# Optimization experiments

Hardware: AMD Instinct MI355X
Metric: run time of the kernel (lower is better)

The kernel has to match this reference:

```python
import jax, jax.numpy as jnp
import numpy as np

NUM_EXPERTS = 32
TOP_K = 4
ALPHA = 1.702   # GPT-OSS GLU alpha
LIMIT = 7.0     # GPT-OSS clamp limit


def setup_inputs() -> dict:
    key = jax.random.key(0)
    ks = jax.random.split(key, 7)
    B, S, H, E = 2, 2048, 1024, NUM_EXPERTS
    return {
        "hidden_states": jax.random.normal(ks[0], (B, S, H), jnp.float32),
        "router_weight": jax.random.normal(ks[1], (E, H), jnp.float32) * 0.02,
        "router_bias": jax.random.normal(ks[2], (E,), jnp.float32) * 0.02,
        "gate_up_proj": jax.random.normal(ks[3], (E, H, 2 * H), jnp.float32) * 0.02,
        "gate_up_proj_bias": jax.random.normal(ks[4], (E, 2 * H), jnp.float32) * 0.02,
        "down_proj": jax.random.normal(ks[5], (E, H, H), jnp.float32) * 0.02,
        "down_proj_bias": jax.random.normal(ks[6], (E, H), jnp.float32) * 0.02,
    }


def _moe_forward(hidden_states, router_weight, router_bias,
                 gate_up_proj, gate_up_proj_bias, down_proj, down_proj_bias):
    B, S, H = hidden_states.shape
    E, K = NUM_EXPERTS, TOP_K
    T = B * S
    capacity = T * K // E * 2  # expert_capacity as in the torch module

    x = hidden_states.reshape(T, H)

    # ---- router: linear -> top-k -> softmax over top-k -> dense scatter ----
    logits = x @ router_weight.T + router_bias                     # [T, E]
    top_vals, top_idx = jax.lax.top_k(logits, K)                   # [T, K]
    weights = jax.nn.softmax(top_vals, axis=-1)                    # [T, K]
    router_scores = jnp.zeros_like(logits).at[
        jnp.arange(T)[:, None], top_idx].set(weights)              # [T, E]

    # ---- capacity-based dispatch (first-come-first-served in token order) ----
    flat_e = top_idx.reshape(-1)                                   # [T*K]
    token_id = jnp.repeat(jnp.arange(T), K)                        # [T*K]
    onehot = (flat_e[:, None] == jnp.arange(E)[None, :]).astype(jnp.int32)
    # rank of each assignment within its expert (0-based, arrival order)
    rank = jnp.take_along_axis(jnp.cumsum(onehot, axis=0),
                               flat_e[:, None], axis=1)[:, 0] - 1  # [T*K]
    valid = rank < capacity
    slot = jnp.where(valid, rank, capacity)  # out-of-range slot -> dropped

    buffer = jnp.zeros((E, capacity, H), x.dtype).at[flat_e, slot].set(
        x[token_id], mode="drop")                                  # [E, C, H]

    # ---- grouped expert MLP: gate_up GEMM + GPT-OSS GLU + down GEMM ----
    gu = jnp.einsum("ech,ehf->ecf", buffer, gate_up_proj) \
         + gate_up_proj_bias[:, None, :]                           # [E, C, 2H]
    gate = gu[..., ::2]
    up = gu[..., 1::2]
    gate = jnp.minimum(gate, LIMIT)
    up = jnp.clip(up, -LIMIT, LIMIT)
    glu = gate * jax.nn.sigmoid(gate * ALPHA)
    act = (up + 1.0) * glu                                         # [E, C, H]
    expert_out = jnp.einsum("ech,ehf->ecf", act, down_proj) \
                 + down_proj_bias[:, None, :]                      # [E, C, H]

    # ---- weighted combine (dropped tokens contribute zero) ----
    gathered = expert_out[flat_e, jnp.where(valid, rank, 0)]       # [T*K, H]
    w = router_scores[token_id, flat_e] * valid.astype(x.dtype)    # [T*K]
    out = jax.ops.segment_sum(gathered * w[:, None], token_id,
                              num_segments=T)                      # [T, H]
    return out.reshape(B, S, H), router_scores


def reference(hidden_states, router_weight, router_bias, gate_up_proj,
              gate_up_proj_bias, down_proj, down_proj_bias):
    return _moe_forward(hidden_states, router_weight, router_bias,
                        gate_up_proj, gate_up_proj_bias, down_proj,
                        down_proj_bias)
```

## Files before the change

kernel.cpp:

```cpp
#include <hip/hip_runtime.h>
#include <hip/hip_bf16.h>

#define T_TOK 4096
#define H_DIM 1024
#define E_EXP 32
#define TOPK 4
#define CAP 1024
#define PAIRS (T_TOK*TOPK)

typedef __attribute__((ext_vector_type(8))) short short8v;
typedef __attribute__((ext_vector_type(4))) short short4v;
typedef __attribute__((ext_vector_type(4))) float f32x4;
typedef unsigned long long u64;
typedef unsigned short ushort;

__device__ __forceinline__ float bf16_bits_to_f32(ushort h) {
    return __uint_as_float(((unsigned)h) << 16);
}
__device__ __forceinline__ unsigned bf16r(float f) {
    unsigned u = __float_as_uint(f);
    return ((u + 0x7fffu + ((u >> 16) & 1u)) >> 16) & 0xffffu;
}
__device__ __forceinline__ unsigned cvt2(float a, float b) {
    unsigned r;
    asm("v_cvt_pk_bf16_f32 %0, %1, %2" : "=v"(r) : "v"(a), "v"(b));
    return r;
}
__device__ __forceinline__ u64 pk4(float a, float b, float c, float d) {
    return (u64)cvt2(a, b) | ((u64)cvt2(c, d) << 32);
}

#define GLD16(gsrc, ldst) \
    __builtin_amdgcn_global_load_lds( \
        (const __attribute__((address_space(1))) unsigned*)(gsrc), \
        (__attribute__((address_space(3))) unsigned*)(ldst), 16, 0, 0)

__global__ __launch_bounds__(256) void router_kernel(
    const float* __restrict__ x, const float* __restrict__ rw,
    const float* __restrict__ rb, float* __restrict__ scores,
    int* __restrict__ flat_e, float* __restrict__ flat_w)
{
    __shared__ float xs[H_DIM];
    __shared__ float lg[E_EXP];
    __shared__ float sw[TOPK];
    __shared__ int   se[TOPK];
    const int t = blockIdx.x;
    const int tid = threadIdx.x;

    for (int i = tid; i < H_DIM; i += 256) xs[i] = x[(size_t)t * H_DIM + i];
    __syncthreads();

    const int e = tid >> 3, l8 = tid & 7;
    float partial = 0.f;
    const float* wr = rw + (size_t)e * H_DIM;
    for (int h = l8; h < H_DIM; h += 8) partial += xs[h] * wr[h];
    partial += __shfl_xor(partial, 1);
    partial += __shfl_xor(partial, 2);
    partial += __shfl_xor(partial, 4);
    if (l8 == 0) lg[e] = partial + rb[e];
    __syncthreads();

    if (tid == 0) {
        unsigned used = 0;
        float bv[TOPK]; int bi[TOPK];
        #pragma unroll
        for (int j = 0; j < TOPK; j++) {
            float best = -1e30f; int bid = -1;
            for (int q = 0; q < E_EXP; q++) {
                if (used & (1u << q)) continue;
                if (lg[q] > best) { best = lg[q]; bid = q; }
            }
            used |= 1u << bid;
            bv[j] = best; bi[j] = bid;
        }
        const float m = bv[0];
        float s = 0.f; float w[TOPK];
        #pragma unroll
        for (int j = 0; j < TOPK; j++) { w[j] = expf(bv[j] - m); s += w[j]; }
        const float inv = 1.f / s;
        #pragma unroll
        for (int j = 0; j < TOPK; j++) { sw[j] = w[j] * inv; se[j] = bi[j]; }
    }
    __syncthreads();

    if (tid < E_EXP) {
        float v = 0.f;
        #pragma unroll
        for (int j = 0; j < TOPK; j++) if (se[j] == tid) v = sw[j];
        scores[(size_t)t * E_EXP + tid] = v;
    }
    if (tid < TOPK) {
        flat_e[t * TOPK + tid] = se[tid];
        flat_w[t * TOPK + tid] = sw[tid];
    }
}

__global__ __launch_bounds__(256) void scan_kernel(
    const int* __restrict__ flat_e, const float* __restrict__ flat_w,
    int* __restrict__ slot_token, float* __restrict__ slot_w,
    int* __restrict__ pair_slot, int* __restrict__ counts)
{
    __shared__ int cnt[256 * E_EXP];
    const int tid = threadIdx.x;
    for (int e = 0; e < E_EXP; e++) cnt[tid * E_EXP + e] = 0;
    __syncthreads();
    const int base = tid * (PAIRS / 256);
    for (int i = 0; i < PAIRS / 256; i++) {
        int e = flat_e[base + i];
        cnt[tid * E_EXP + e]++;
    }
    __syncthreads();
    if (tid < E_EXP) {
        int run = 0;
        for (int i = 0; i < 256; i++) {
            int idx = i * E_EXP + tid;
            int v = cnt[idx];
            cnt[idx] = run;
            run += v;
        }
        counts[tid] = min(run, CAP);
    }
    __syncthreads();
    for (int i = 0; i < PAIRS / 256; i++) {
        int p = base + i;
        int e = flat_e[p];
        int r = cnt[tid * E_EXP + e]++;
        if (r < CAP) {
            slot_token[e * CAP + r] = p >> 2;
            slot_w[e * CAP + r] = flat_w[p];
            pair_slot[p] = r;
        } else {
            pair_slot[p] = -1;
        }
    }
}

__global__ __launch_bounds__(256) void stage_tokens(
    const float* __restrict__ x, const int* __restrict__ slot_token,
    const int* __restrict__ counts, char* __restrict__ xbuf)
{
    const int e = blockIdx.y, rt = blockIdx.x;
    const int n = counts[e];
    const int row0 = rt * 128;
    if (row0 >= n) return;
    const int rows_here = min(128, n - row0);
    const int lane = threadIdx.x & 63, wv = threadIdx.x >> 6;
    char* tb = xbuf + ((size_t)(e * 8 + rt)) * 262144;

    for (int r = wv; r < rows_here; r += 4) {
        const float* xr = x + (size_t)slot_token[e * CAP + row0 + r] * H_DIM;
        #pragma unroll
        for (int q = 0; q < 2; ++q) {
            int g = q * 64 + lane;
            float4 a = *(const float4*)(xr + g * 8);
            float4 b = *(const float4*)(xr + g * 8 + 4);
            uint4 w;
            w.x = cvt2(a.x, a.y); w.y = cvt2(a.z, a.w);
            w.z = cvt2(b.x, b.y); w.w = cvt2(b.z, b.w);
            int kb = g >> 2, gi = g & 3;
            *(uint4*)(tb + kb * 8192 + r * 64 + ((gi ^ (r & 3)) * 16)) = w;
        }
    }
}

__global__ __launch_bounds__(256, 3) void gateup_mfma(
    const char* __restrict__ xbuf,
    const float* __restrict__ wgu,
    const float* __restrict__ gub,
    const int* __restrict__ counts,
    char* __restrict__ act)
{
    const int lin = blockIdx.x;
    const int xcd = lin & 7, slot = lin >> 3;
    const int gg = (slot >> 3) * 8 + xcd;
    const int rt = slot & 7;
    const int e = gg >> 4, ct = gg & 15;

    const int n = counts[e];
    const int row0 = rt * 128;
    if (row0 >= n) return;
    const int rows_here = min(128, n - row0);
    const int c0f = ct * 64, c0gu = ct * 128;

    __shared__ char AsB[2][8192];
    __shared__ char BgB[2][4096];
    __shared__ char BuB[2][4096];

    const int tid = threadIdx.x;
    const int lane = tid & 63, wid = tid >> 6;
    const int wr = wid >> 1, wc = wid & 1;
    const int l15 = lane & 15, l4 = lane >> 4;

    const char* xtile = xbuf + ((size_t)(e * 8 + rt)) * 262144;

    f32x4 accg[4][2], accu[4][2];
    #pragma unroll
    for (int m = 0; m < 4; m++)
        #pragma unroll
        for (int j = 0; j < 2; j++) { accg[m][j] = (f32x4)0.f; accu[m][j] = (f32x4)0.f; }

    float2 bgv[2][4];
    const int bnp = tid & 63;
    const int bkq0 = tid >> 6;

    auto stageA = [&](int buf, int t) {
        const char* src = xtile + (size_t)t * 8192 + wid * 2048 + lane * 16;
        char* dst = AsB[buf] + wid * 2048;
        GLD16(src, dst);
        GLD16(src + 1024, dst + 1024);
    };
    auto bload = [&](int k0) {
        #pragma unroll
        for (int u = 0; u < 2; ++u) {
            int kq = bkq0 + 4 * u;
            const float* src = wgu + ((size_t)e * H_DIM + k0 + kq * 4) * 2048 + c0gu + 2 * bnp;
            #pragma unroll
            for (int q = 0; q < 4; ++q) bgv[u][q] = *(const float2*)(src + (size_t)q * 2048);
        }
    };
    auto bpack = [&](int buf) {
        #pragma unroll
        for (int u = 0; u < 2; ++u) {
            int kq = bkq0 + 4 * u;
            *(u64*)(BgB[buf] + kq * 512 + bnp * 8) =
                pk4(bgv[u][0].x, bgv[u][1].x, bgv[u][2].x, bgv[u][3].x);
            *(u64*)(BuB[buf] + kq * 512 + bnp * 8) =
                pk4(bgv[u][0].y, bgv[u][1].y, bgv[u][2].y, bgv[u][3].y);
        }
    };

    bload(0);
    stageA(0, 0);
    bpack(0);
    __syncthreads();
    int cur = 0;

    for (int t = 0; t < 32; ++t) {
        if (t < 31) { bload((t + 1) * 32); stageA(cur ^ 1, t + 1); }

        short8v afr[4];
        #pragma unroll
        for (int m = 0; m < 4; ++m) {
            int row = wr * 64 + m * 16 + l15;
            afr[m] = *(short8v*)(AsB[cur] + row * 64 + ((l4 ^ (row & 3)) * 16));
        }
        #pragma unroll
        for (int j = 0; j < 2; ++j) {
            int f = wc * 32 + j * 16 + l15;
            short4v glo = *(short4v*)(BgB[cur] + (2 * l4) * 512 + f * 8);
            short4v ghi = *(short4v*)(BgB[cur] + (2 * l4 + 1) * 512 + f * 8);
            short4v ulo = *(short4v*)(BuB[cur] + (2 * l4) * 512 + f * 8);
            short4v uhi = *(short4v*)(BuB[cur] + (2 * l4 + 1) * 512 + f * 8);
            short8v bg8 = __builtin_shufflevector(glo, ghi, 0, 1, 2, 3, 4, 5, 6, 7);
            short8v bu8 = __builtin_shufflevector(ulo, uhi, 0, 1, 2, 3, 4, 5, 6, 7);
            #pragma unroll
            for (int m = 0; m < 4; ++m) {
                accg[m][j] = __builtin_amdgcn_mfma_f32_16x16x32_bf16(afr[m], bg8, accg[m][j], 0, 0, 0);
                accu[m][j] = __builtin_amdgcn_mfma_f32_16x16x32_bf16(afr[m], bu8, accu[m][j], 0, 0, 0);
            }
        }
        if (t < 31) bpack(cur ^ 1);
        __syncthreads();
        cur ^= 1;
    }

    char* atile = act + ((size_t)(e * 8 + rt)) * 262144;
    #pragma unroll
    for (int j = 0; j < 2; ++j) {
        int f = c0f + wc * 32 + j * 16 + l15;
        float bgb = gub[(size_t)e * 2048 + 2 * f];
        float bub = gub[(size_t)e * 2048 + 2 * f + 1];
        int kb = f >> 5, gi = (f & 31) >> 3, ke = f & 7;
        #pragma unroll
        for (int m = 0; m < 4; ++m) {
            int rbase = wr * 64 + m * 16 + l4 * 4;
            #pragma unroll
            for (int reg = 0; reg < 4; ++reg) {
                int r = rbase + reg;
                if (r >= rows_here) continue;
                float g = accg[m][j][reg] + bgb;
                float u = accu[m][j][reg] + bub;
                g = fminf(g, 7.0f);
                u = fminf(fmaxf(u, -7.0f), 7.0f);
                float glu = g / (1.0f + __expf(-1.702f * g));
                float a = (u + 1.0f) * glu;
                *(ushort*)(atile + kb * 8192 + r * 64 + ((gi ^ (r & 3)) * 16) + ke * 2)
                    = (ushort)bf16r(a);
            }
        }
    }
}

__global__ __launch_bounds__(256, 3) void down_mfma(
    const char* __restrict__ act,
    const float* __restrict__ wd,
    const float* __restrict__ db,
    const int* __restrict__ counts,
    ushort* __restrict__ eout)
{
    const int lin = blockIdx.x;
    const int xcd = lin & 7, slot = lin >> 3;
    const int gg = (slot >> 3) * 8 + xcd;
    const int rt = slot & 7;
    const int e = gg >> 3, ct = gg & 7;

    const int n = counts[e];
    const int row0 = rt * 128;
    if (row0 >= n) return;
    const int rows_here = min(128, n - row0);
    const int c0 = ct * 128;

    __shared__ char AsB[2][8192];
    __shared__ char BsB[2][8192];

    const int tid = threadIdx.x;
    const int lane = tid & 63, wid = tid >> 6;
    const int wr = wid >> 1, wc = wid & 1;
    const int l15 = lane & 15, l4 = lane >> 4;

    const char* atile = act + ((size_t)(e * 8 + rt)) * 262144;

    f32x4 acc[4][4];
    #pragma unroll
    for (int m = 0; m < 4; m++)
        #pragma unroll
        for (int j = 0; j < 4; j++) acc[m][j] = (f32x4)0.f;

    float2 bvd[2][4];
    const int bnp = tid & 63;
    const int bkq0 = tid >> 6;

    auto stageA = [&](int buf, int t) {
        const char* src = atile + (size_t)t * 8192 + wid * 2048 + lane * 16;
        char* dst = AsB[buf] + wid * 2048;
        GLD16(src, dst);
        GLD16(src + 1024, dst + 1024);
    };
    auto bload = [&](int k0) {
        #pragma unroll
        for (int u = 0; u < 2; ++u) {
            int kq = bkq0 + 4 * u;
            const float* src = wd + ((size_t)e * H_DIM + k0 + kq * 4) * H_DIM + c0 + 2 * bnp;
            #pragma unroll
            for (int q = 0; q < 4; ++q) bvd[u][q] = *(const float2*)(src + (size_t)q * H_DIM);
        }
    };
    auto bpack = [&](int buf) {
        #pragma unroll
        for (int u = 0; u < 2; ++u) {
            int kq = bkq0 + 4 * u;
            char* dst = BsB[buf] + kq * 1024 + bnp * 16;
            *(u64*)dst       = pk4(bvd[u][0].x, bvd[u][1].x, bvd[u][2].x, bvd[u][3].x);
            *(u64*)(dst + 8) = pk4(bvd[u][0].y, bvd[u][1].y, bvd[u][2].y, bvd[u][3].y);
        }
    };

    bload(0);
    stageA(0, 0);
    bpack(0);
    __syncthreads();
    int cur = 0;

    for (int t = 0; t < 32; ++t) {
        if (t < 31) { bload((t + 1) * 32); stageA(cur ^ 1, t + 1); }

        short8v afr[4];
        #pragma unroll
        for (int m = 0; m < 4; ++m) {
            int row = wr * 64 + m * 16 + l15;
            afr[m] = *(short8v*)(AsB[cur] + row * 64 + ((l4 ^ (row & 3)) * 16));
        }
        #pragma unroll
        for (int j = 0; j < 4; ++j) {
            int nn = wc * 64 + j * 16 + l15;
            short4v lo = *(short4v*)(BsB[cur] + (2 * l4) * 1024 + nn * 8);
            short4v hi = *(short4v*)(BsB[cur] + (2 * l4 + 1) * 1024 + nn * 8);
            short8v b8 = __builtin_shufflevector(lo, hi, 0, 1, 2, 3, 4, 5, 6, 7);
            #pragma unroll
            for (int m = 0; m < 4; ++m)
                acc[m][j] = __builtin_amdgcn_mfma_f32_16x16x32_bf16(afr[m], b8, acc[m][j], 0, 0, 0);
        }
        if (t < 31) bpack(cur ^ 1);
        __syncthreads();
        cur ^= 1;
    }

    #pragma unroll
    for (int j = 0; j < 4; ++j) {
        int col = c0 + wc * 64 + j * 16 + l15;
        float bias = db[(size_t)e * H_DIM + col];
        #pragma unroll
        for (int m = 0; m < 4; ++m) {
            int rbase = wr * 64 + m * 16 + l4 * 4;
            #pragma unroll
            for (int reg = 0; reg < 4; ++reg) {
                int r = rbase + reg;
                if (r >= rows_here) continue;
                eout[((size_t)e * CAP + row0 + r) * H_DIM + col] =
                    (ushort)bf16r(acc[m][j][reg] + bias);
            }
        }
    }
}

__global__ __launch_bounds__(256) void finalize_kernel(
    const ushort* __restrict__ eout, const int* __restrict__ flat_e,
    const float* __restrict__ flat_w, const int* __restrict__ pair_slot,
    float* __restrict__ out)
{
    const int t = blockIdx.x;
    const int c = threadIdx.x * 4;
    float a0 = 0.f, a1 = 0.f, a2 = 0.f, a3 = 0.f;
    #pragma unroll
    for (int k = 0; k < TOPK; ++k) {
        int p = t * TOPK + k;
        int s = pair_slot[p];
        if (s < 0) continue;
        int e = flat_e[p];
        float w = flat_w[p];
        const ushort* row = eout + ((size_t)e * CAP + s) * H_DIM + c;
        ushort4 v = *(const ushort4*)row;
        a0 += w * bf16_bits_to_f32(v.x);
        a1 += w * bf16_bits_to_f32(v.y);
        a2 += w * bf16_bits_to_f32(v.z);
        a3 += w * bf16_bits_to_f32(v.w);
    }
    *(float4*)(out + (size_t)t * H_DIM + c) = make_float4(a0, a1, a2, a3);
}

extern "C" void kernel_launch(void* const* d_in, const int* in_sizes, int n_in,
                              void* d_out, int out_size, void* d_ws, size_t ws_size,
                              hipStream_t stream) {
    const float* x   = (const float*)d_in[0];
    const float* rw  = (const float*)d_in[1];
    const float* rb  = (const float*)d_in[2];
    const float* wgu = (const float*)d_in[3];
    const float* gub = (const float*)d_in[4];
    const float* wd  = (const float*)d_in[5];
    const float* db  = (const float*)d_in[6];

    float* out    = (float*)d_out;
    float* scores = out + (size_t)T_TOK * H_DIM;

    char* ws = (char*)d_ws;
    char* xbuf = ws;
    ushort* eout = (ushort*)ws;
    size_t off = (size_t)E_EXP * CAP * H_DIM * 2;
    char* act = ws + off;          off += (size_t)E_EXP * CAP * H_DIM * 2;
    int*   flat_e     = (int*)(ws + off);   off += PAIRS * 4;
    float* flat_w     = (float*)(ws + off); off += PAIRS * 4;
    int*   slot_token = (int*)(ws + off);   off += E_EXP * CAP * 4;
    float* slot_w     = (float*)(ws + off); off += E_EXP * CAP * 4;
    int*   pair_slot  = (int*)(ws + off);   off += PAIRS * 4;
    int*   counts     = (int*)(ws + off);   off += E_EXP * 4;
    (void)ws_size; (void)out_size; (void)n_in; (void)in_sizes; (void)slot_w;

    hipLaunchKernelGGL(router_kernel, dim3(T_TOK), dim3(256), 0, stream,
                       x, rw, rb, scores, flat_e, flat_w);
    hipLaunchKernelGGL(scan_kernel, dim3(1), dim3(256), 0, stream,
                       flat_e, flat_w, slot_token, slot_w, pair_slot, counts);
    hipLaunchKernelGGL(stage_tokens, dim3(8, E_EXP), dim3(256), 0, stream,
                       x, slot_token, counts, xbuf);
    hipLaunchKernelGGL(gateup_mfma, dim3(4096), dim3(256), 0, stream,
                       xbuf, wgu, gub, counts, act);
    hipLaunchKernelGGL(down_mfma, dim3(2048), dim3(256), 0, stream,
                       act, wd, db, counts, eout);
    hipLaunchKernelGGL(finalize_kernel, dim3(T_TOK), dim3(256), 0, stream,
                       eout, flat_e, flat_w, pair_slot, out);
}
```

Before: 494.4 us.

## Pre-convert expert weights to bf16 tiled layout and stage via direct LDS loads

Adds conv_gu and conv_dn kernels that convert the fp32 gate_up and down weights into pre-swizzled bf16 tiles in a workspace buffer, split into two halves of experts for gate_up to bound workspace size. The GEMM kernels then stage the B operand with global_load_lds, dropping the per-tile register load, convert and pack steps, and read B fragments with a single 16-byte LDS load. The A-side swizzle changes to (row>>1)&3. The cost is extra launches and a full pass over the weights (read fp32, write bf16), which happens every call and includes tiles for experts with no tokens.

```diff
diff --git a/kernel.cpp b/kernel.cpp
--- a/kernel.cpp
+++ b/kernel.cpp
@@ -9,7 +9,6 @@
 #define PAIRS (T_TOK*TOPK)
 
 typedef __attribute__((ext_vector_type(8))) short short8v;
-typedef __attribute__((ext_vector_type(4))) short short4v;
 typedef __attribute__((ext_vector_type(4))) float f32x4;
 typedef unsigned long long u64;
 typedef unsigned short ushort;
@@ -25,9 +24,6 @@
     unsigned r;
     asm("v_cvt_pk_bf16_f32 %0, %1, %2" : "=v"(r) : "v"(a), "v"(b));
     return r;
-}
-__device__ __forceinline__ u64 pk4(float a, float b, float c, float d) {
-    return (u64)cvt2(a, b) | ((u64)cvt2(c, d) << 32);
 }
 
 #define GLD16(gsrc, ldst) \
@@ -149,42 +145,96 @@
 
     for (int r = wv; r < rows_here; r += 4) {
         const float* xr = x + (size_t)slot_token[e * CAP + row0 + r] * H_DIM;
-        #pragma unroll
-        for (int q = 0; q < 2; ++q) {
-            int g = q * 64 + lane;
-            float4 a = *(const float4*)(xr + g * 8);
-            float4 b = *(const float4*)(xr + g * 8 + 4);
+        const int s = (r >> 1) & 3;
+        #pragma unroll
+        for (int half = 0; half < 2; ++half) {
+            int gi = half * 64 + lane;
+            float4 a = *(const float4*)(xr + gi * 8);
+            float4 b = *(const float4*)(xr + gi * 8 + 4);
             uint4 w;
             w.x = cvt2(a.x, a.y); w.y = cvt2(a.z, a.w);
             w.z = cvt2(b.x, b.y); w.w = cvt2(b.z, b.w);
-            int kb = g >> 2, gi = g & 3;
-            *(uint4*)(tb + kb * 8192 + r * 64 + ((gi ^ (r & 3)) * 16)) = w;
-        }
+            int t = gi >> 2, kq = gi & 3;
+            *(uint4*)(tb + (size_t)t * 8192 + r * 64 + ((kq ^ s) * 16)) = w;
+        }
+    }
+}
+
+__global__ __launch_bounds__(256) void conv_gu(
+    const float* __restrict__ wgu, char* __restrict__ wbuf, int e_base)
+{
+    const int ct = blockIdx.x;
+    const int tseg = blockIdx.y;
+    const int el = blockIdx.z;
+    const int e = e_base + el;
+    const int lane = threadIdx.x & 63, wv = threadIdx.x >> 6;
+    char* dst_base = wbuf + ((size_t)(el * 16 + ct) * 32) * 8192;
+    #pragma unroll
+    for (int i = 0; i < 2; ++i) {
+        const int t = tseg * 8 + wv * 2 + i;
+        const float* src = wgu + ((size_t)e * 1024 + t * 32) * 2048 + ct * 128 + 2 * lane;
+        float2 v[32];
+        #pragma unroll
+        for (int k = 0; k < 32; ++k) v[k] = *(const float2*)(src + (size_t)k * 2048);
+        char* dst = dst_base + (size_t)t * 8192 + lane * 16;
+        #pragma unroll
+        for (int kq = 0; kq < 4; ++kq) {
+            uint4 g, u;
+            g.x = cvt2(v[kq*8+0].x, v[kq*8+1].x); g.y = cvt2(v[kq*8+2].x, v[kq*8+3].x);
+            g.z = cvt2(v[kq*8+4].x, v[kq*8+5].x); g.w = cvt2(v[kq*8+6].x, v[kq*8+7].x);
+            u.x = cvt2(v[kq*8+0].y, v[kq*8+1].y); u.y = cvt2(v[kq*8+2].y, v[kq*8+3].y);
+            u.z = cvt2(v[kq*8+4].y, v[kq*8+5].y); u.w = cvt2(v[kq*8+6].y, v[kq*8+7].y);
+            *(uint4*)(dst + kq * 1024) = g;
+            *(uint4*)(dst + 4096 + kq * 1024) = u;
+        }
+    }
+}
+
+__global__ __launch_bounds__(256) void conv_dn(
+    const float* __restrict__ wd, char* __restrict__ wbuf)
+{
+    const int ct = blockIdx.x;
+    const int tseg = blockIdx.y;
+    const int e = blockIdx.z;
+    const int lane = threadIdx.x & 63, wv = threadIdx.x >> 6;
+    const int t = tseg * 4 + wv;
+    const float* src = wd + ((size_t)e * 1024 + t * 32) * 1024 + ct * 128 + 2 * lane;
+    float2 v[32];
+    #pragma unroll
+    for (int k = 0; k < 32; ++k) v[k] = *(const float2*)(src + (size_t)k * 1024);
+    char* dst = wbuf + (((size_t)(e * 8 + ct) * 32) + t) * 8192 + (2 * lane) * 16;
+    #pragma unroll
+    for (int kq = 0; kq < 4; ++kq) {
+        uint4 g0, g1;
+        g0.x = cvt2(v[kq*8+0].x, v[kq*8+1].x); g0.y = cvt2(v[kq*8+2].x, v[kq*8+3].x);
+        g0.z = cvt2(v[kq*8+4].x, v[kq*8+5].x); g0.w = cvt2(v[kq*8+6].x, v[kq*8+7].x);
+        g1.x = cvt2(v[kq*8+0].y, v[kq*8+1].y); g1.y = cvt2(v[kq*8+2].y, v[kq*8+3].y);
+        g1.z = cvt2(v[kq*8+4].y, v[kq*8+5].y); g1.w = cvt2(v[kq*8+6].y, v[kq*8+7].y);
+        *(uint4*)(dst + kq * 2048) = g0;
+        *(uint4*)(dst + kq * 2048 + 16) = g1;
     }
 }
 
 __global__ __launch_bounds__(256, 3) void gateup_mfma(
-    const char* __restrict__ xbuf,
-    const float* __restrict__ wgu,
-    const float* __restrict__ gub,
-    const int* __restrict__ counts,
-    char* __restrict__ act)
+    const char* __restrict__ xbuf, const char* __restrict__ wbuf,
+    const float* __restrict__ gub, const int* __restrict__ counts,
+    char* __restrict__ act, int e_base)
 {
     const int lin = blockIdx.x;
     const int xcd = lin & 7, slot = lin >> 3;
     const int gg = (slot >> 3) * 8 + xcd;
     const int rt = slot & 7;
-    const int e = gg >> 4, ct = gg & 15;
+    const int el = gg >> 4, ct = gg & 15;
+    const int e = e_base + el;
 
     const int n = counts[e];
     const int row0 = rt * 128;
     if (row0 >= n) return;
     const int rows_here = min(128, n - row0);
-    const int c0f = ct * 64, c0gu = ct * 128;
+    const int c0f = ct * 64;
 
     __shared__ char AsB[2][8192];
-    __shared__ char BgB[2][4096];
-    __shared__ char BuB[2][4096];
+    __shared__ char BsB[2][8192];
 
     const int tid = threadIdx.x;
     const int lane = tid & 63, wid = tid >> 6;
@@ -192,6 +242,7 @@
     const int l15 = lane & 15, l4 = lane >> 4;
 
     const char* xtile = xbuf + ((size_t)(e * 8 + rt)) * 262144;
+    const char* btile = wbuf + ((size_t)(el * 16 + ct) * 32) * 8192;
 
     f32x4 accg[4][2], accu[4][2];
     #pragma unroll
@@ -199,67 +250,38 @@
         #pragma unroll
         for (int j = 0; j < 2; j++) { accg[m][j] = (f32x4)0.f; accu[m][j] = (f32x4)0.f; }
 
-    float2 bgv[2][4];
-    const int bnp = tid & 63;
-    const int bkq0 = tid >> 6;
-
-    auto stageA = [&](int buf, int t) {
-        const char* src = xtile + (size_t)t * 8192 + wid * 2048 + lane * 16;
-        char* dst = AsB[buf] + wid * 2048;
-        GLD16(src, dst);
-        GLD16(src + 1024, dst + 1024);
+    auto stage = [&](int buf, int t) {
+        const char* sa = xtile + (size_t)t * 8192 + tid * 16;
+        GLD16(sa, AsB[buf] + tid * 16);
+        GLD16(sa + 4096, AsB[buf] + 4096 + tid * 16);
+        const char* sb = btile + (size_t)t * 8192 + tid * 16;
+        GLD16(sb, BsB[buf] + tid * 16);
+        GLD16(sb + 4096, BsB[buf] + 4096 + tid * 16);
     };
-    auto bload = [&](int k0) {
-        #pragma unroll
-        for (int u = 0; u < 2; ++u) {
-            int kq = bkq0 + 4 * u;
-            const float* src = wgu + ((size_t)e * H_DIM + k0 + kq * 4) * 2048 + c0gu + 2 * bnp;
-            #pragma unroll
-            for (int q = 0; q < 4; ++q) bgv[u][q] = *(const float2*)(src + (size_t)q * 2048);
-        }
-    };
-    auto bpack = [&](int buf) {
-        #pragma unroll
-        for (int u = 0; u < 2; ++u) {
-            int kq = bkq0 + 4 * u;
-            *(u64*)(BgB[buf] + kq * 512 + bnp * 8) =
-                pk4(bgv[u][0].x, bgv[u][1].x, bgv[u][2].x, bgv[u][3].x);
-            *(u64*)(BuB[buf] + kq * 512 + bnp * 8) =
-                pk4(bgv[u][0].y, bgv[u][1].y, bgv[u][2].y, bgv[u][3].y);
-        }
-    };
-
-    bload(0);
-    stageA(0, 0);
-    bpack(0);
+
+    stage(0, 0);
     __syncthreads();
     int cur = 0;
-
     for (int t = 0; t < 32; ++t) {
-        if (t < 31) { bload((t + 1) * 32); stageA(cur ^ 1, t + 1); }
+        if (t < 31) stage(cur ^ 1, t + 1);
 
         short8v afr[4];
         #pragma unroll
         for (int m = 0; m < 4; ++m) {
             int row = wr * 64 + m * 16 + l15;
-            afr[m] = *(short8v*)(AsB[cur] + row * 64 + ((l4 ^ (row & 3)) * 16));
+            afr[m] = *(short8v*)(AsB[cur] + row * 64 + ((l4 ^ ((row >> 1) & 3)) * 16));
         }
         #pragma unroll
         for (int j = 0; j < 2; ++j) {
-            int f = wc * 32 + j * 16 + l15;
-            short4v glo = *(short4v*)(BgB[cur] + (2 * l4) * 512 + f * 8);
-            short4v ghi = *(short4v*)(BgB[cur] + (2 * l4 + 1) * 512 + f * 8);
-            short4v ulo = *(short4v*)(BuB[cur] + (2 * l4) * 512 + f * 8);
-            short4v uhi = *(short4v*)(BuB[cur] + (2 * l4 + 1) * 512 + f * 8);
-            short8v bg8 = __builtin_shufflevector(glo, ghi, 0, 1, 2, 3, 4, 5, 6, 7);
-            short8v bu8 = __builtin_shufflevector(ulo, uhi, 0, 1, 2, 3, 4, 5, 6, 7);
+            int fl = wc * 32 + j * 16 + l15;
+            short8v bg8 = *(short8v*)(BsB[cur] + l4 * 1024 + fl * 16);
+            short8v bu8 = *(short8v*)(BsB[cur] + 4096 + l4 * 1024 + fl * 16);
             #pragma unroll
             for (int m = 0; m < 4; ++m) {
                 accg[m][j] = __builtin_amdgcn_mfma_f32_16x16x32_bf16(afr[m], bg8, accg[m][j], 0, 0, 0);
                 accu[m][j] = __builtin_amdgcn_mfma_f32_16x16x32_bf16(afr[m], bu8, accu[m][j], 0, 0, 0);
             }
         }
-        if (t < 31) bpack(cur ^ 1);
         __syncthreads();
         cur ^= 1;
     }
@@ -270,7 +292,7 @@
         int f = c0f + wc * 32 + j * 16 + l15;
         float bgb = gub[(size_t)e * 2048 + 2 * f];
         float bub = gub[(size_t)e * 2048 + 2 * f + 1];
-        int kb = f >> 5, gi = (f & 31) >> 3, ke = f & 7;
+        int tt = f >> 5, kq = (f & 31) >> 3, ke = f & 7;
         #pragma unroll
         for (int m = 0; m < 4; ++m) {
             int rbase = wr * 64 + m * 16 + l4 * 4;
@@ -284,18 +306,16 @@
                 u = fminf(fmaxf(u, -7.0f), 7.0f);
                 float glu = g / (1.0f + __expf(-1.702f * g));
                 float a = (u + 1.0f) * glu;
-                *(ushort*)(atile + kb * 8192 + r * 64 + ((gi ^ (r & 3)) * 16) + ke * 2)
-                    = (ushort)bf16r(a);
+                *(ushort*)(atile + (size_t)tt * 8192 + r * 64 +
+                           ((kq ^ ((r >> 1) & 3)) * 16) + ke * 2) = (ushort)bf16r(a);
             }
         }
     }
 }
 
 __global__ __launch_bounds__(256, 3) void down_mfma(
-    const char* __restrict__ act,
-    const float* __restrict__ wd,
-    const float* __restrict__ db,
-    const int* __restrict__ counts,
+    const char* __restrict__ act, const char* __restrict__ wbuf,
+    const float* __restrict__ db, const int* __restrict__ counts,
     ushort* __restrict__ eout)
 {
     const int lin = blockIdx.x;
@@ -319,6 +339,7 @@
     const int l15 = lane & 15, l4 = lane >> 4;
 
     const char* atile = act + ((size_t)(e * 8 + rt)) * 262144;
+    const char* btile = wbuf + ((size_t)(e * 8 + ct) * 32) * 8192;
 
     f32x4 acc[4][4];
     #pragma unroll
@@ -326,61 +347,35 @@
         #pragma unroll
         for (int j = 0; j < 4; j++) acc[m][j] = (f32x4)0.f;
 
-    float2 bvd[2][4];
-    const int bnp = tid & 63;
-    const int bkq0 = tid >> 6;
-
-    auto stageA = [&](int buf, int t) {
-        const char* src = atile + (size_t)t * 8192 + wid * 2048 + lane * 16;
-        char* dst = AsB[buf] + wid * 2048;
-        GLD16(src, dst);
-        GLD16(src + 1024, dst + 1024);
+    auto stage = [&](int buf, int t) {
+        const char* sa = atile + (size_t)t * 8192 + tid * 16;
+        GLD16(sa, AsB[buf] + tid * 16);
+        GLD16(sa + 4096, AsB[buf] + 4096 + tid * 16);
+        const char* sb = btile + (size_t)t * 8192 + tid * 16;
+        GLD16(sb, BsB[buf] + tid * 16);
+        GLD16(sb + 4096, BsB[buf] + 4096 + tid * 16);
     };
-    auto bload = [&](int k0) {
-        #pragma unroll
-        for (int u = 0; u < 2; ++u) {
-            int kq = bkq0 + 4 * u;
-            const float* src = wd + ((size_t)e * H_DIM + k0 + kq * 4) * H_DIM + c0 + 2 * bnp;
-            #pragma unroll
-            for (int q = 0; q < 4; ++q) bvd[u][q] = *(const float2*)(src + (size_t)q * H_DIM);
-        }
-    };
-    auto bpack = [&](int buf) {
-        #pragma unroll
-        for (int u = 0; u < 2; ++u) {
-            int kq = bkq0 + 4 * u;
-            char* dst = BsB[buf] + kq * 1024 + bnp * 16;
-            *(u64*)dst       = pk4(bvd[u][0].x, bvd[u][1].x, bvd[u][2].x, bvd[u][3].x);
-            *(u64*)(dst + 8) = pk4(bvd[u][0].y, bvd[u][1].y, bvd[u][2].y, bvd[u][3].y);
-        }
-    };
-
-    bload(0);
-    stageA(0, 0);
-    bpack(0);
+
+    stage(0, 0);
     __syncthreads();
     int cur = 0;
-
     for (int t = 0; t < 32; ++t) {
-        if (t < 31) { bload((t + 1) * 32); stageA(cur ^ 1, t + 1); }
+        if (t < 31) stage(cur ^ 1, t + 1);
 
         short8v afr[4];
         #pragma unroll
         for (int m = 0; m < 4; ++m) {
             int row = wr * 64 + m * 16 + l15;
-            afr[m] = *(short8v*)(AsB[cur] + row * 64 + ((l4 ^ (row & 3)) * 16));
+            afr[m] = *(short8v*)(AsB[cur] + row * 64 + ((l4 ^ ((row >> 1) & 3)) * 16));
         }
         #pragma unroll
         for (int j = 0; j < 4; ++j) {
             int nn = wc * 64 + j * 16 + l15;
-            short4v lo = *(short4v*)(BsB[cur] + (2 * l4) * 1024 + nn * 8);
-            short4v hi = *(short4v*)(BsB[cur] + (2 * l4 + 1) * 1024 + nn * 8);
-            short8v b8 = __builtin_shufflevector(lo, hi, 0, 1, 2, 3, 4, 5, 6, 7);
+            short8v b8 = *(short8v*)(BsB[cur] + l4 * 2048 + nn * 16);
             #pragma unroll
             for (int m = 0; m < 4; ++m)
                 acc[m][j] = __builtin_amdgcn_mfma_f32_16x16x32_bf16(afr[m], b8, acc[m][j], 0, 0, 0);
         }
-        if (t < 31) bpack(cur ^ 1);
         __syncthreads();
         cur ^= 1;
     }
@@ -446,7 +441,8 @@
     char* xbuf = ws;
     ushort* eout = (ushort*)ws;
     size_t off = (size_t)E_EXP * CAP * H_DIM * 2;
-    char* act = ws + off;          off += (size_t)E_EXP * CAP * H_DIM * 2;
+    char* act  = ws + off;  off += (size_t)E_EXP * CAP * H_DIM * 2;
+    char* wbuf = ws + off;  off += (size_t)16 * 16 * 32 * 8192;
     int*   flat_e     = (int*)(ws + off);   off += PAIRS * 4;
     float* flat_w     = (float*)(ws + off); off += PAIRS * 4;
     int*   slot_token = (int*)(ws + off);   off += E_EXP * CAP * 4;
@@ -461,10 +457,15 @@
                        flat_e, flat_w, slot_token, slot_w, pair_slot, counts);
     hipLaunchKernelGGL(stage_tokens, dim3(8, E_EXP), dim3(256), 0, stream,
                        x, slot_token, counts, xbuf);
-    hipLaunchKernelGGL(gateup_mfma, dim3(4096), dim3(256), 0, stream,
-                       xbuf, wgu, gub, counts, act);
+    hipLaunchKernelGGL(conv_gu, dim3(16, 4, 16), dim3(256), 0, stream, wgu, wbuf, 0);
+    hipLaunchKernelGGL(gateup_mfma, dim3(2048), dim3(256), 0, stream,
+                       xbuf, wbuf, gub, counts, act, 0);
+    hipLaunchKernelGGL(conv_gu, dim3(16, 4, 16), dim3(256), 0, stream, wgu, wbuf, 16);
+    hipLaunchKernelGGL(gateup_mfma, dim3(2048), dim3(256), 0, stream,
+                       xbuf, wbuf, gub, counts, act, 16);
+    hipLaunchKernelGGL(conv_dn, dim3(8, 8, 32), dim3(256), 0, stream, wd, wbuf);
     hipLaunchKernelGGL(down_mfma, dim3(2048), dim3(256), 0, stream,
-                       act, wd, db, counts, eout);
+                       act, wbuf, db, counts, eout);
     hipLaunchKernelGGL(finalize_kernel, dim3(T_TOK), dim3(256), 0, stream,
                        eout, flat_e, flat_w, pair_slot, out);
 }
```

Measured after the change: 521.6 us. +5.5%, slower.

## Deepen weight prefetch pipeline and rework LDS layouts in MoE MFMA GEMMs

Applied to the files above, without the earlier changes.

Both expert GEMM kernels now prefetch weight tiles two K-steps ahead using alternating register buffers, with explicit vmcnt waits, sched barriers and raw s_barrier in place of __syncthreads. The B-tile LDS layout is changed so each lane reads one 16-byte fragment instead of two 8-byte halves plus a shuffle. The A-tile swizzle is changed to (row>>1)&3 in the staging, gate-up epilogue and fragment reads, and MFMA sections are wrapped in s_setprio. This aims to hide global weight-load latency and cut LDS instruction count and bank conflicts, at the cost of more registers and hand-tuned wait counts that must match the issued load counts exactly.

```diff
diff --git a/kernel.cpp b/kernel.cpp
--- a/kernel.cpp
+++ b/kernel.cpp
@@ -9,7 +9,6 @@
 #define PAIRS (T_TOK*TOPK)
 
 typedef __attribute__((ext_vector_type(8))) short short8v;
-typedef __attribute__((ext_vector_type(4))) short short4v;
 typedef __attribute__((ext_vector_type(4))) float f32x4;
 typedef unsigned long long u64;
 typedef unsigned short ushort;
@@ -34,6 +33,11 @@
     __builtin_amdgcn_global_load_lds( \
         (const __attribute__((address_space(1))) unsigned*)(gsrc), \
         (__attribute__((address_space(3))) unsigned*)(ldst), 16, 0, 0)
+
+#define WAIT_VM(N)   asm volatile("s_waitcnt vmcnt(" #N ")" ::: "memory")
+#define WAIT_VMLG(N) asm volatile("s_waitcnt vmcnt(" #N ") lgkmcnt(0)" ::: "memory")
+#define SCHEDB()     __builtin_amdgcn_sched_barrier(0)
+#define BARRIER()    __builtin_amdgcn_s_barrier()
 
 __global__ __launch_bounds__(256) void router_kernel(
     const float* __restrict__ x, const float* __restrict__ rw,
@@ -149,25 +153,24 @@
 
     for (int r = wv; r < rows_here; r += 4) {
         const float* xr = x + (size_t)slot_token[e * CAP + row0 + r] * H_DIM;
-        #pragma unroll
-        for (int q = 0; q < 2; ++q) {
-            int g = q * 64 + lane;
-            float4 a = *(const float4*)(xr + g * 8);
-            float4 b = *(const float4*)(xr + g * 8 + 4);
+        const int s = (r >> 1) & 3;
+        #pragma unroll
+        for (int half = 0; half < 2; ++half) {
+            int gi = half * 64 + lane;
+            float4 a = *(const float4*)(xr + gi * 8);
+            float4 b = *(const float4*)(xr + gi * 8 + 4);
             uint4 w;
             w.x = cvt2(a.x, a.y); w.y = cvt2(a.z, a.w);
             w.z = cvt2(b.x, b.y); w.w = cvt2(b.z, b.w);
-            int kb = g >> 2, gi = g & 3;
-            *(uint4*)(tb + kb * 8192 + r * 64 + ((gi ^ (r & 3)) * 16)) = w;
+            int t = gi >> 2, kq = gi & 3;
+            *(uint4*)(tb + (size_t)t * 8192 + r * 64 + ((kq ^ s) * 16)) = w;
         }
     }
 }
 
 __global__ __launch_bounds__(256, 3) void gateup_mfma(
-    const char* __restrict__ xbuf,
-    const float* __restrict__ wgu,
-    const float* __restrict__ gub,
-    const int* __restrict__ counts,
+    const char* __restrict__ xbuf, const float* __restrict__ wgu,
+    const float* __restrict__ gub, const int* __restrict__ counts,
     char* __restrict__ act)
 {
     const int lin = blockIdx.x;
@@ -190,6 +193,7 @@
     const int lane = tid & 63, wid = tid >> 6;
     const int wr = wid >> 1, wc = wid & 1;
     const int l15 = lane & 15, l4 = lane >> 4;
+    const int bnp = tid & 63, bkq0 = tid >> 6;
 
     const char* xtile = xbuf + ((size_t)(e * 8 + rt)) * 262144;
 
@@ -199,70 +203,86 @@
         #pragma unroll
         for (int j = 0; j < 2; j++) { accg[m][j] = (f32x4)0.f; accu[m][j] = (f32x4)0.f; }
 
-    float2 bgv[2][4];
-    const int bnp = tid & 63;
-    const int bkq0 = tid >> 6;
+    float2 bv0[8], bv1[8];
+    int cur = 0;
 
     auto stageA = [&](int buf, int t) {
-        const char* src = xtile + (size_t)t * 8192 + wid * 2048 + lane * 16;
-        char* dst = AsB[buf] + wid * 2048;
-        GLD16(src, dst);
-        GLD16(src + 1024, dst + 1024);
-    };
-    auto bload = [&](int k0) {
+        const char* sa = xtile + (size_t)t * 8192 + tid * 16;
+        GLD16(sa, AsB[buf] + tid * 16);
+        GLD16(sa + 4096, AsB[buf] + 4096 + tid * 16);
+    };
+    auto bload = [&](float2 (&ld)[8], int t) {
+        #pragma unroll
+        for (int u = 0; u < 2; ++u) {
+            const float* src = wgu + ((size_t)e * 1024 + t * 32 + (bkq0 + 4 * u) * 4) * 2048
+                               + c0gu + 2 * bnp;
+            #pragma unroll
+            for (int q = 0; q < 4; ++q) ld[u * 4 + q] = *(const float2*)(src + (size_t)q * 2048);
+        }
+    };
+    auto bpack = [&](int buf, float2 (&pk)[8]) {
         #pragma unroll
         for (int u = 0; u < 2; ++u) {
             int kq = bkq0 + 4 * u;
-            const float* src = wgu + ((size_t)e * H_DIM + k0 + kq * 4) * 2048 + c0gu + 2 * bnp;
-            #pragma unroll
-            for (int q = 0; q < 4; ++q) bgv[u][q] = *(const float2*)(src + (size_t)q * 2048);
-        }
-    };
-    auto bpack = [&](int buf) {
-        #pragma unroll
-        for (int u = 0; u < 2; ++u) {
-            int kq = bkq0 + 4 * u;
-            *(u64*)(BgB[buf] + kq * 512 + bnp * 8) =
-                pk4(bgv[u][0].x, bgv[u][1].x, bgv[u][2].x, bgv[u][3].x);
-            *(u64*)(BuB[buf] + kq * 512 + bnp * 8) =
-                pk4(bgv[u][0].y, bgv[u][1].y, bgv[u][2].y, bgv[u][3].y);
-        }
-    };
-
-    bload(0);
-    stageA(0, 0);
-    bpack(0);
-    __syncthreads();
-    int cur = 0;
-
-    for (int t = 0; t < 32; ++t) {
-        if (t < 31) { bload((t + 1) * 32); stageA(cur ^ 1, t + 1); }
-
+            char* dg = BgB[buf] + (kq >> 1) * 1024 + bnp * 16 + (kq & 1) * 8;
+            char* du = BuB[buf] + (kq >> 1) * 1024 + bnp * 16 + (kq & 1) * 8;
+            *(u64*)dg = pk4(pk[u*4+0].x, pk[u*4+1].x, pk[u*4+2].x, pk[u*4+3].x);
+            *(u64*)du = pk4(pk[u*4+0].y, pk[u*4+1].y, pk[u*4+2].y, pk[u*4+3].y);
+        }
+    };
+    auto compute = [&]() {
         short8v afr[4];
         #pragma unroll
         for (int m = 0; m < 4; ++m) {
             int row = wr * 64 + m * 16 + l15;
-            afr[m] = *(short8v*)(AsB[cur] + row * 64 + ((l4 ^ (row & 3)) * 16));
-        }
+            afr[m] = *(short8v*)(AsB[cur] + row * 64 + ((l4 ^ ((row >> 1) & 3)) * 16));
+        }
+        __builtin_amdgcn_s_setprio(1);
         #pragma unroll
         for (int j = 0; j < 2; ++j) {
-            int f = wc * 32 + j * 16 + l15;
-            short4v glo = *(short4v*)(BgB[cur] + (2 * l4) * 512 + f * 8);
-            short4v ghi = *(short4v*)(BgB[cur] + (2 * l4 + 1) * 512 + f * 8);
-            short4v ulo = *(short4v*)(BuB[cur] + (2 * l4) * 512 + f * 8);
-            short4v uhi = *(short4v*)(BuB[cur] + (2 * l4 + 1) * 512 + f * 8);
-            short8v bg8 = __builtin_shufflevector(glo, ghi, 0, 1, 2, 3, 4, 5, 6, 7);
-            short8v bu8 = __builtin_shufflevector(ulo, uhi, 0, 1, 2, 3, 4, 5, 6, 7);
+            int fl = wc * 32 + j * 16 + l15;
+            short8v bg8 = *(short8v*)(BgB[cur] + l4 * 1024 + fl * 16);
+            short8v bu8 = *(short8v*)(BuB[cur] + l4 * 1024 + fl * 16);
             #pragma unroll
             for (int m = 0; m < 4; ++m) {
                 accg[m][j] = __builtin_amdgcn_mfma_f32_16x16x32_bf16(afr[m], bg8, accg[m][j], 0, 0, 0);
                 accu[m][j] = __builtin_amdgcn_mfma_f32_16x16x32_bf16(afr[m], bu8, accu[m][j], 0, 0, 0);
             }
         }
-        if (t < 31) bpack(cur ^ 1);
-        __syncthreads();
-        cur ^= 1;
-    }
+        __builtin_amdgcn_s_setprio(0);
+    };
+
+    stageA(0, 0);
+    bload(bv0, 0);
+    bload(bv1, 1);
+    WAIT_VM(8); SCHEDB();
+    bpack(0, bv0);
+    WAIT_VMLG(8); SCHEDB();
+    BARRIER(); SCHEDB();
+
+    #define GU_ITER(T, LD, PK) { \
+        stageA(cur ^ 1, (T) + 1); \
+        bload(LD, (T) + 2); \
+        compute(); SCHEDB(); \
+        WAIT_VM(10); SCHEDB(); \
+        bpack(cur ^ 1, PK); \
+        WAIT_VMLG(8); SCHEDB(); \
+        BARRIER(); SCHEDB(); \
+        cur ^= 1; }
+
+    for (int t = 0; t < 30; t += 2) {
+        GU_ITER(t, bv0, bv1);
+        GU_ITER(t + 1, bv1, bv0);
+    }
+    #undef GU_ITER
+    stageA(cur ^ 1, 31);
+    compute(); SCHEDB();
+    WAIT_VM(2); SCHEDB();
+    bpack(cur ^ 1, bv1);
+    WAIT_VMLG(0); SCHEDB();
+    BARRIER(); SCHEDB();
+    cur ^= 1;
+    compute();
 
     char* atile = act + ((size_t)(e * 8 + rt)) * 262144;
     #pragma unroll
@@ -270,7 +290,7 @@
         int f = c0f + wc * 32 + j * 16 + l15;
         float bgb = gub[(size_t)e * 2048 + 2 * f];
         float bub = gub[(size_t)e * 2048 + 2 * f + 1];
-        int kb = f >> 5, gi = (f & 31) >> 3, ke = f & 7;
+        int tt = f >> 5, kq = (f & 31) >> 3, ke = f & 7;
         #pragma unroll
         for (int m = 0; m < 4; ++m) {
             int rbase = wr * 64 + m * 16 + l4 * 4;
@@ -284,18 +304,16 @@
                 u = fminf(fmaxf(u, -7.0f), 7.0f);
                 float glu = g / (1.0f + __expf(-1.702f * g));
                 float a = (u + 1.0f) * glu;
-                *(ushort*)(atile + kb * 8192 + r * 64 + ((gi ^ (r & 3)) * 16) + ke * 2)
-                    = (ushort)bf16r(a);
+                *(ushort*)(atile + (size_t)tt * 8192 + r * 64 +
+                           ((kq ^ ((r >> 1) & 3)) * 16) + ke * 2) = (ushort)bf16r(a);
             }
         }
     }
 }
 
 __global__ __launch_bounds__(256, 3) void down_mfma(
-    const char* __restrict__ act,
-    const float* __restrict__ wd,
-    const float* __restrict__ db,
-    const int* __restrict__ counts,
+    const char* __restrict__ act, const float* __restrict__ wd,
+    const float* __restrict__ db, const int* __restrict__ counts,
     ushort* __restrict__ eout)
 {
     const int lin = blockIdx.x;
@@ -317,6 +335,7 @@
     const int lane = tid & 63, wid = tid >> 6;
     const int wr = wid >> 1, wc = wid & 1;
     const int l15 = lane & 15, l4 = lane >> 4;
+    const int bnp = tid & 63, bkq0 = tid >> 6;
 
     const char* atile = act + ((size_t)(e * 8 + rt)) * 262144;
 
@@ -326,64 +345,82 @@
         #pragma unroll
         for (int j = 0; j < 4; j++) acc[m][j] = (f32x4)0.f;
 
-    float2 bvd[2][4];
-    const int bnp = tid & 63;
-    const int bkq0 = tid >> 6;
+    float2 bv0[8], bv1[8];
+    int cur = 0;
 
     auto stageA = [&](int buf, int t) {
-        const char* src = atile + (size_t)t * 8192 + wid * 2048 + lane * 16;
-        char* dst = AsB[buf] + wid * 2048;
-        GLD16(src, dst);
-        GLD16(src + 1024, dst + 1024);
-    };
-    auto bload = [&](int k0) {
+        const char* sa = atile + (size_t)t * 8192 + tid * 16;
+        GLD16(sa, AsB[buf] + tid * 16);
+        GLD16(sa + 4096, AsB[buf] + 4096 + tid * 16);
+    };
+    auto bload = [&](float2 (&ld)[8], int t) {
+        #pragma unroll
+        for (int u = 0; u < 2; ++u) {
+            const float* src = wd + ((size_t)e * 1024 + t * 32 + (bkq0 + 4 * u) * 4) * 1024
+                               + c0 + 2 * bnp;
+            #pragma unroll
+            for (int q = 0; q < 4; ++q) ld[u * 4 + q] = *(const float2*)(src + (size_t)q * 1024);
+        }
+    };
+    auto bpack = [&](int buf, float2 (&pk)[8]) {
         #pragma unroll
         for (int u = 0; u < 2; ++u) {
             int kq = bkq0 + 4 * u;
-            const float* src = wd + ((size_t)e * H_DIM + k0 + kq * 4) * H_DIM + c0 + 2 * bnp;
-            #pragma unroll
-            for (int q = 0; q < 4; ++q) bvd[u][q] = *(const float2*)(src + (size_t)q * H_DIM);
-        }
-    };
-    auto bpack = [&](int buf) {
-        #pragma unroll
-        for (int u = 0; u < 2; ++u) {
-            int kq = bkq0 + 4 * u;
-            char* dst = BsB[buf] + kq * 1024 + bnp * 16;
-            *(u64*)dst       = pk4(bvd[u][0].x, bvd[u][1].x, bvd[u][2].x, bvd[u][3].x);
-            *(u64*)(dst + 8) = pk4(bvd[u][0].y, bvd[u][1].y, bvd[u][2].y, bvd[u][3].y);
-        }
-    };
-
-    bload(0);
-    stageA(0, 0);
-    bpack(0);
-    __syncthreads();
-    int cur = 0;
-
-    for (int t = 0; t < 32; ++t) {
-        if (t < 31) { bload((t + 1) * 32); stageA(cur ^ 1, t + 1); }
-
+            char* d0 = BsB[buf] + (kq >> 1) * 2048 + (2 * bnp) * 16 + (kq & 1) * 8;
+            *(u64*)d0        = pk4(pk[u*4+0].x, pk[u*4+1].x, pk[u*4+2].x, pk[u*4+3].x);
+            *(u64*)(d0 + 16) = pk4(pk[u*4+0].y, pk[u*4+1].y, pk[u*4+2].y, pk[u*4+3].y);
+        }
+    };
+    auto compute = [&]() {
         short8v afr[4];
         #pragma unroll
         for (int m = 0; m < 4; ++m) {
             int row = wr * 64 + m * 16 + l15;
-            afr[m] = *(short8v*)(AsB[cur] + row * 64 + ((l4 ^ (row & 3)) * 16));
-        }
+            afr[m] = *(short8v*)(AsB[cur] + row * 64 + ((l4 ^ ((row >> 1) & 3)) * 16));
+        }
+        __builtin_amdgcn_s_setprio(1);
         #pragma unroll
         for (int j = 0; j < 4; ++j) {
             int nn = wc * 64 + j * 16 + l15;
-            short4v lo = *(short4v*)(BsB[cur] + (2 * l4) * 1024 + nn * 8);
-            short4v hi = *(short4v*)(BsB[cur] + (2 * l4 + 1) * 1024 + nn * 8);
-            short8v b8 = __builtin_shufflevector(lo, hi, 0, 1, 2, 3, 4, 5, 6, 7);
+            short8v b8 = *(short8v*)(BsB[cur] + l4 * 2048 + nn * 16);
             #pragma unroll
             for (int m = 0; m < 4; ++m)
                 acc[m][j] = __builtin_amdgcn_mfma_f32_16x16x32_bf16(afr[m], b8, acc[m][j], 0, 0, 0);
         }
-        if (t < 31) bpack(cur ^ 1);
-        __syncthreads();
-        cur ^= 1;
-    }
+        __builtin_amdgcn_s_setprio(0);
+    };
+
+    stageA(0, 0);
+    bload(bv0, 0);
+    bload(bv1, 1);
+    WAIT_VM(8); SCHEDB();
+    bpack(0, bv0);
+    WAIT_VMLG(8); SCHEDB();
+    BARRIER(); SCHEDB();
+
+    #define DN_ITER(T, LD, PK) { \
+        stageA(cur ^ 1, (T) + 1); \
+        bload(LD, (T) + 2); \
+        compute(); SCHEDB(); \
+        WAIT_VM(10); SCHEDB(); \
+        bpack(cur ^ 1, PK); \
+        WAIT_VMLG(8); SCHEDB(); \
+        BARRIER(); SCHEDB(); \
+        cur ^= 1; }
+
+    for (int t = 0; t < 30; t += 2) {
+        DN_ITER(t, bv0, bv1);
+        DN_ITER(t + 1, bv1, bv0);
+    }
+    #undef DN_ITER
+    stageA(cur ^ 1, 31);
+    compute(); SCHEDB();
+    WAIT_VM(2); SCHEDB();
+    bpack(cur ^ 1, bv1);
+    WAIT_VMLG(0); SCHEDB();
+    BARRIER(); SCHEDB();
+    cur ^= 1;
+    compute();
 
     #pragma unroll
     for (int j = 0; j < 4; ++j) {
@@ -446,7 +483,7 @@
     char* xbuf = ws;
     ushort* eout = (ushort*)ws;
     size_t off = (size_t)E_EXP * CAP * H_DIM * 2;
-    char* act = ws + off;          off += (size_t)E_EXP * CAP * H_DIM * 2;
+    char* act  = ws + off;  off += (size_t)E_EXP * CAP * H_DIM * 2;
     int*   flat_e     = (int*)(ws + off);   off += PAIRS * 4;
     float* flat_w     = (float*)(ws + off); off += PAIRS * 4;
     int*   slot_token = (int*)(ws + off);   off += E_EXP * CAP * 4;
```

Result: faster. 478.3 us (-3.3%).
